# Performance work log

Hardware: AMD Instinct MI355X
Metric: run time of the kernel (lower is better)

The kernel has to match this reference:

```python
import jax, jax.numpy as jnp
import numpy as np

K = 16          # number of discrete value bins (values in [0, K))
EPOCHS = 200.0  # self.epochs in the module


def _mi_from_joint(joint):
    # sklearn mutual_info_score from a KxK contingency table (natural log)
    n = joint.sum()
    pij = joint / n
    pi = pij.sum(axis=1, keepdims=True)
    pj = pij.sum(axis=0, keepdims=True)
    safe_log = lambda p: jnp.log(jnp.where(p > 0, p, 1.0))
    terms = pij * (safe_log(pij) - safe_log(pi) - safe_log(pj))
    return jnp.where(pij > 0, terms, 0.0).sum()


def _pair_mi(a, b):
    # a, b: int32 vectors of equal length; histogram-based MI
    idx = a * K + b
    joint = jnp.zeros(K * K, jnp.float32).at[idx].add(1.0).reshape(K, K)
    return _mi_from_joint(joint)


def _mi_mask(x):
    # x: (b, t, c, h, w) float with integer values in [0, K)
    b, t, c, h, w = x.shape
    s = x.astype(jnp.int32).transpose(1, 0, 2, 3, 4).reshape(t, b * c, h * w)
    s0 = s[0]
    # global MI between t=0 and each t, over all b*c*h*w samples
    glob = jax.vmap(lambda st: _pair_mi(s0.reshape(-1), st.reshape(-1)))(s)  # (t,)
    # per-spatial-element MI between t=0 and each t, over b*c samples
    ele = jax.vmap(jax.vmap(_pair_mi, in_axes=(1, 1)), in_axes=(None, 0))(s0, s)  # (t, hw)
    mi = ele * glob[:, None]
    mi = mi / mi[0]          # divide every row by row 0 (broadcast over t)
    mi = mi.at[0].set(0.0)
    return mi.reshape(t, h, w)


def setup_inputs() -> dict:
    key = jax.random.key(0)
    k1, k2 = jax.random.split(key)
    b, t, c, h, w = 16, 8, 32, 64, 64
    x = jax.random.randint(k1, (b, t, c, h, w), 0, K).astype(jnp.float32)
    noise = jax.random.uniform(k2, (b, t, c, h, w), dtype=jnp.float32)
    return {"x": x, "noise": noise, "epoch": 50}


def reference(x, noise, epoch):
    mi = _mi_mask(x)                                   # (t, h, w)
    prob = jnp.clip(mi * (epoch / EPOCHS), 0.0, 1.0)
    mask = noise < prob[None, :, None, :, :]           # (b,t,c,h,w)
    return jnp.where(mask, 0.0, x)
```

## Files before the change

### kernel.cpp

```cpp
#include <hip/hip_runtime.h>
#include <math.h>

#define B_   16
#define T_   8
#define C_   32
#define HW_  4096
#define K_   16
#define CHW_ (C_*HW_)
#define BC_  (B_*C_)
#define P_BLK 8

typedef unsigned int uint;

__global__ __launch_bounds__(256) void k_pack(const float4* __restrict__ x4,
                                              uint4* __restrict__ packed4) {
  const int n  = blockIdx.x * 256 + threadIdx.x;
  const int bc = n >> 10;
  const int p4 = n & 1023;
  const int b  = bc >> 5;
  const int c  = bc & 31;
  uint4 acc = make_uint4(0u, 0u, 0u, 0u);
  #pragma unroll
  for (int t = 0; t < T_; ++t) {
    const float4 xv = x4[((b * T_ + t) * C_ + c) * (HW_ / 4) + p4];
    const int sh = 4 * t;
    acc.x |= ((uint)xv.x) << sh;
    acc.y |= ((uint)xv.y) << sh;
    acc.z |= ((uint)xv.z) << sh;
    acc.w |= ((uint)xv.w) << sh;
  }
  packed4[n] = acc;
}

__global__ __launch_bounds__(512) void k_hist_mi(const uint* __restrict__ packed,
                                                 uint* __restrict__ glob_hist,
                                                 double* __restrict__ ele) {
  __shared__ uint   hist[T_][P_BLK][256];
  __shared__ double logtab[513];

  const int tid = threadIdx.x;
  const int p0  = blockIdx.x * P_BLK;

  for (int i = tid; i < T_ * P_BLK * 256; i += 512) ((uint*)hist)[i] = 0u;
  for (int i = tid; i < 513; i += 512) logtab[i] = (i > 0) ? log((double)i) : 0.0;
  __syncthreads();

  const int lp  = tid & 7;
  const int g   = tid >> 3;
  const int rot = lp * 37;

  uint w[8];
  #pragma unroll
  for (int k = 0; k < 8; ++k)
    w[k] = packed[(g + (k << 6)) * HW_ + p0 + lp];

  #pragma unroll
  for (int k = 0; k < 8; ++k) {
    const uint wk  = w[k];
    const int  a   = (int)(wk & 15u);
    const int  row = a << 4;
    atomicAdd(&hist[0][lp][((row | a) + rot) & 255], 1u);
    #pragma unroll
    for (int t = 1; t < T_; ++t) {
      const int v = (int)((wk >> (4 * t)) & 15u);
      atomicAdd(&hist[t][lp][((row | v) + rot) & 255], 1u);
    }
  }
  __syncthreads();

  for (int i = tid; i < T_ * 256; i += 512) {
    const int t = i >> 8, bin = i & 255;
    uint s = 0;
    #pragma unroll
    for (int p = 0; p < P_BLK; ++p) s += hist[t][p][(bin + p * 37) & 255];
    atomicAdd(&glob_hist[i], s);
  }

  if (tid < T_ * P_BLK) {
    const int t    = tid >> 3;
    const int lpp  = tid & 7;
    const int rr   = lpp * 37;
    const uint* h  = &hist[t][lpp][0];
    double term = 0.0;
    #pragma unroll
    for (int a = 0; a < K_; ++a) {
      uint r = 0;
      #pragma unroll
      for (int v = 0; v < K_; ++v) {
        const uint cnt = h[(((a << 4) | v) + rr) & 255];
        r += cnt;
        term += (double)cnt * logtab[cnt];
      }
      term -= (double)r * logtab[r];
    }
    #pragma unroll
    for (int v = 0; v < K_; ++v) {
      uint col = 0;
      #pragma unroll
      for (int a = 0; a < K_; ++a) col += h[(((a << 4) | v) + rr) & 255];
      term -= (double)col * logtab[col];
    }
    ele[t * HW_ + p0 + lpp] = logtab[512] + term * (1.0 / 512.0);
  }
}

__global__ __launch_bounds__(256) void k_glob(const uint* __restrict__ glob_hist,
                                              double* __restrict__ glob) {
  __shared__ double part[256];
  const int tid = threadIdx.x;

  if (tid < 128) {
    const int t = tid >> 4, a = tid & 15;
    const uint* h = glob_hist + t * 256 + (a << 4);
    double s = 0.0, r = 0.0;
    #pragma unroll
    for (int v = 0; v < K_; ++v) {
      const double cnt = (double)h[v];
      r += cnt;
      if (cnt > 0.0) s += cnt * log(cnt);
    }
    if (r > 0.0) s -= r * log(r);
    part[tid] = s;
  } else {
    const int t = (tid - 128) >> 4, v = (tid - 128) & 15;
    const uint* h = glob_hist + t * 256 + v;
    double col = 0.0;
    #pragma unroll
    for (int a = 0; a < K_; ++a) col += (double)h[a << 4];
    part[tid] = (col > 0.0) ? -col * log(col) : 0.0;
  }
  __syncthreads();

  if (tid < T_) {
    double term = 0.0;
    #pragma unroll
    for (int i = 0; i < 16; ++i)
      term += part[tid * 16 + i] + part[128 + tid * 16 + i];
    const double n = (double)BC_ * (double)HW_;
    glob[tid] = log(n) + term / n;
  }
}

__global__ __launch_bounds__(256) void k_prob(const double* __restrict__ ele,
                                              const double* __restrict__ glob,
                                              const int* __restrict__ epoch_ptr,
                                              float* __restrict__ prob) {
  const int i = blockIdx.x * 256 + threadIdx.x;
  const int t = i >> 12;
  const int p = i & (HW_ - 1);
  float pv;
  if (t == 0) {
    pv = 0.0f;
  } else {
    const double escale = (double)(*epoch_ptr) * (1.0 / 200.0);
    const double mi0 = ele[p] * glob[0];
    const double mit = ele[i] * glob[t];
    const double v  = (mit / mi0) * escale;
    pv = fminf(fmaxf((float)v, 0.0f), 1.0f);
  }
  prob[i] = pv;
}

__global__ __launch_bounds__(256) void k_mask(const float4* __restrict__ x4,
                                              const float4* __restrict__ n4,
                                              const float* __restrict__ prob,
                                              float4* __restrict__ o4) {
  const int i = blockIdx.x * 256 + threadIdx.x;
  const int t = (i >> 15) & 7;
  const float4 pr = ((const float4*)prob)[(t << 10) | (i & 1023)];
  const float4 xv = x4[i];
  const float4 nv = n4[i];
  float4 o;
  o.x = (nv.x < pr.x) ? 0.0f : xv.x;
  o.y = (nv.y < pr.y) ? 0.0f : xv.y;
  o.z = (nv.z < pr.z) ? 0.0f : xv.z;
  o.w = (nv.w < pr.w) ? 0.0f : xv.w;
  o4[i] = o;
}

extern "C" void kernel_launch(void* const* d_in, const int* in_sizes, int n_in,
                              void* d_out, int out_size, void* d_ws, size_t ws_size,
                              hipStream_t stream) {
  const float* x     = (const float*)d_in[0];
  const float* noise = (const float*)d_in[1];
  const int*   epoch = (const int*)d_in[2];
  float*       out   = (float*)d_out;

  char* ws = (char*)d_ws;
  uint*   glob_hist = (uint*)ws;
  uint*   packed    = (uint*)(ws + 8192);
  double* ele       = (double*)(ws + 8192 + (size_t)BC_ * HW_ * 4);
  double* glob      = (double*)((char*)ele + (size_t)T_ * HW_ * 8);
  float*  prob      = (float*)((char*)glob + 64);

  hipMemsetAsync(glob_hist, 0, 8192, stream);

  k_pack<<<(BC_ * HW_ / 4) / 256, 256, 0, stream>>>((const float4*)x,
                                                    (uint4*)packed);
  k_hist_mi<<<HW_ / P_BLK, 512, 0, stream>>>(packed, glob_hist, ele);
  k_glob<<<1, 256, 0, stream>>>(glob_hist, glob);
  k_prob<<<(T_ * HW_) / 256, 256, 0, stream>>>(ele, glob, epoch, prob);

  const int n4 = (B_ * T_ * C_ * HW_) / 4;
  k_mask<<<n4 / 256, 256, 0, stream>>>((const float4*)x, (const float4*)noise,
                                       prob, (float4*)out);
}
```

Before: 212.6 us.

## Reuse packed nibbles in mask, fuse glob/prob, parallelize per-element MI

The mask kernel now reads the 4-bit packed tensor instead of re-reading full float x, which cuts roughly a third of the mask pass's global traffic. The glob and prob kernels are merged, with glob recomputed redundantly in each of the 32 blocks. The histogram memset is folded into the pack kernel. Per-element MI entropy is now spread across all 512 threads using wave shuffle reductions instead of 64 serial threads. This trades slightly more redundant compute for fewer launches and less bandwidth.

```diff
diff --git a/kernel.cpp b/kernel.cpp
--- a/kernel.cpp
+++ b/kernel.cpp
@@ -6,15 +6,21 @@
 #define C_   32
 #define HW_  4096
 #define K_   16
-#define CHW_ (C_*HW_)
 #define BC_  (B_*C_)
 #define P_BLK 8
 
 typedef unsigned int uint;
 
 __global__ __launch_bounds__(256) void k_pack(const float4* __restrict__ x4,
-                                              uint4* __restrict__ packed4) {
-  const int n  = blockIdx.x * 256 + threadIdx.x;
+                                              uint4* __restrict__ packed4,
+                                              uint4* __restrict__ glob_hist4) {
+  const int tid = threadIdx.x;
+  if (blockIdx.x == 0) {
+    const uint4 z = make_uint4(0u, 0u, 0u, 0u);
+    glob_hist4[tid] = z;
+    glob_hist4[tid + 256] = z;
+  }
+  const int n  = blockIdx.x * 256 + tid;
   const int bc = n >> 10;
   const int p4 = n & 1023;
   const int b  = bc >> 5;
@@ -76,37 +82,43 @@
     atomicAdd(&glob_hist[i], s);
   }
 
-  if (tid < T_ * P_BLK) {
-    const int t    = tid >> 3;
-    const int lpp  = tid & 7;
-    const int rr   = lpp * 37;
-    const uint* h  = &hist[t][lpp][0];
-    double term = 0.0;
-    #pragma unroll
-    for (int a = 0; a < K_; ++a) {
+  const int wid  = tid >> 6;
+  const int lane = tid & 63;
+  #pragma unroll
+  for (int p = 0; p < P_BLK; ++p) {
+    const uint* h = &hist[wid][p][0];
+    const int   rr = p * 37;
+    double acc = 0.0;
+    #pragma unroll
+    for (int j0 = 0; j0 < 4; ++j0) {
+      const uint cnt = h[((lane << 2) + j0 + rr) & 255];
+      acc += (double)cnt * logtab[cnt];
+    }
+    if (lane < 16) {
       uint r = 0;
       #pragma unroll
-      for (int v = 0; v < K_; ++v) {
-        const uint cnt = h[(((a << 4) | v) + rr) & 255];
-        r += cnt;
-        term += (double)cnt * logtab[cnt];
-      }
-      term -= (double)r * logtab[r];
-    }
-    #pragma unroll
-    for (int v = 0; v < K_; ++v) {
+      for (int v = 0; v < K_; ++v) r += h[(((lane << 4) | v) + rr) & 255];
+      acc -= (double)r * logtab[r];
+    } else if (lane < 32) {
+      const int v = lane - 16;
       uint col = 0;
       #pragma unroll
       for (int a = 0; a < K_; ++a) col += h[(((a << 4) | v) + rr) & 255];
-      term -= (double)col * logtab[col];
-    }
-    ele[t * HW_ + p0 + lpp] = logtab[512] + term * (1.0 / 512.0);
-  }
-}
-
-__global__ __launch_bounds__(256) void k_glob(const uint* __restrict__ glob_hist,
-                                              double* __restrict__ glob) {
+      acc -= (double)col * logtab[col];
+    }
+    #pragma unroll
+    for (int m = 1; m < 64; m <<= 1) acc += __shfl_xor(acc, m, 64);
+    if (lane == 0)
+      ele[wid * HW_ + p0 + p] = logtab[512] + acc * (1.0 / 512.0);
+  }
+}
+
+__global__ __launch_bounds__(256) void k_glob_prob(const uint* __restrict__ glob_hist,
+                                                   const double* __restrict__ ele,
+                                                   const int* __restrict__ epoch_ptr,
+                                                   float* __restrict__ prob) {
   __shared__ double part[256];
+  __shared__ double glob[T_];
   const int tid = threadIdx.x;
 
   if (tid < 128) {
@@ -139,36 +151,44 @@
     const double n = (double)BC_ * (double)HW_;
     glob[tid] = log(n) + term / n;
   }
-}
-
-__global__ __launch_bounds__(256) void k_prob(const double* __restrict__ ele,
-                                              const double* __restrict__ glob,
-                                              const int* __restrict__ epoch_ptr,
-                                              float* __restrict__ prob) {
-  const int i = blockIdx.x * 256 + threadIdx.x;
-  const int t = i >> 12;
-  const int p = i & (HW_ - 1);
-  float pv;
-  if (t == 0) {
-    pv = 0.0f;
-  } else {
-    const double escale = (double)(*epoch_ptr) * (1.0 / 200.0);
-    const double mi0 = ele[p] * glob[0];
-    const double mit = ele[i] * glob[t];
-    const double v  = (mit / mi0) * escale;
-    pv = fminf(fmaxf((float)v, 0.0f), 1.0f);
-  }
-  prob[i] = pv;
-}
-
-__global__ __launch_bounds__(256) void k_mask(const float4* __restrict__ x4,
+  __syncthreads();
+
+  const double escale = (double)(*epoch_ptr) * (1.0 / 200.0);
+  #pragma unroll
+  for (int k = 0; k < 4; ++k) {
+    const int i = blockIdx.x * 1024 + k * 256 + tid;
+    const int t = i >> 12;
+    const int p = i & (HW_ - 1);
+    float pv = 0.0f;
+    if (t != 0) {
+      const double mi0 = ele[p] * glob[0];
+      const double mit = ele[i] * glob[t];
+      const double v  = (mit / mi0) * escale;
+      pv = fminf(fmaxf((float)v, 0.0f), 1.0f);
+    }
+    prob[i] = pv;
+  }
+}
+
+__global__ __launch_bounds__(256) void k_mask(const uint4* __restrict__ packed4,
                                               const float4* __restrict__ n4,
                                               const float* __restrict__ prob,
                                               float4* __restrict__ o4) {
-  const int i = blockIdx.x * 256 + threadIdx.x;
-  const int t = (i >> 15) & 7;
-  const float4 pr = ((const float4*)prob)[(t << 10) | (i & 1023)];
-  const float4 xv = x4[i];
+  const int i  = blockIdx.x * 256 + threadIdx.x;
+  const int p4 = i & 1023;
+  const int tc = i >> 10;
+  const int c  = tc & 31;
+  const int bt = tc >> 5;
+  const int t  = bt & 7;
+  const int b  = bt >> 3;
+  const uint4 pk = packed4[(((b << 5) | c) << 10) | p4];
+  const int sh = 4 * t;
+  float4 xv;
+  xv.x = (float)((pk.x >> sh) & 15u);
+  xv.y = (float)((pk.y >> sh) & 15u);
+  xv.z = (float)((pk.z >> sh) & 15u);
+  xv.w = (float)((pk.w >> sh) & 15u);
+  const float4 pr = ((const float4*)prob)[(t << 10) | p4];
   const float4 nv = n4[i];
   float4 o;
   o.x = (nv.x < pr.x) ? 0.0f : xv.x;
@@ -190,18 +210,16 @@
   uint*   glob_hist = (uint*)ws;
   uint*   packed    = (uint*)(ws + 8192);
   double* ele       = (double*)(ws + 8192 + (size_t)BC_ * HW_ * 4);
-  double* glob      = (double*)((char*)ele + (size_t)T_ * HW_ * 8);
-  float*  prob      = (float*)((char*)glob + 64);
-
-  hipMemsetAsync(glob_hist, 0, 8192, stream);
+  float*  prob      = (float*)((char*)ele + (size_t)T_ * HW_ * 8);
 
   k_pack<<<(BC_ * HW_ / 4) / 256, 256, 0, stream>>>((const float4*)x,
-                                                    (uint4*)packed);
+                                                    (uint4*)packed,
+                                                    (uint4*)glob_hist);
   k_hist_mi<<<HW_ / P_BLK, 512, 0, stream>>>(packed, glob_hist, ele);
-  k_glob<<<1, 256, 0, stream>>>(glob_hist, glob);
-  k_prob<<<(T_ * HW_) / 256, 256, 0, stream>>>(ele, glob, epoch, prob);
+  k_glob_prob<<<32, 256, 0, stream>>>(glob_hist, ele, epoch, prob);
 
   const int n4 = (B_ * T_ * C_ * HW_) / 4;
-  k_mask<<<n4 / 256, 256, 0, stream>>>((const float4*)x, (const float4*)noise,
+  k_mask<<<n4 / 256, 256, 0, stream>>>((const uint4*)packed,
+                                       (const float4*)noise,
                                        prob, (float4*)out);
 }
```

Measured after the change: 208.8 us. About the same (-1.8%).
